# Kernel tuning notes

Measured on AMD Instinct MI355X. Metric: run time of the kernel, lower is better.

The kernel has to match this reference:

```python
import jax, jax.numpy as jnp
import numpy as np

N = 200000
E = 3200000
C = 64


def setup_inputs() -> dict:
    key = jax.random.key(0)
    ks = jax.random.split(key, 7)
    x = jax.random.normal(ks[0], (N, C), dtype=jnp.float32)
    sources = jax.random.randint(ks[1], (E,), 0, N, dtype=jnp.int32)
    targets = jax.random.randint(ks[2], (E,), 0, N, dtype=jnp.int32)
    norm = jax.random.uniform(ks[3], (N, 1), dtype=jnp.float32)
    norm_t = jax.random.uniform(ks[4], (N, 1), dtype=jnp.float32)
    # xavier_normal for [64,64] Linear: std = sqrt(2/(fan_in+fan_out))
    std = np.sqrt(2.0 / (C + C)).astype(np.float32)
    W_out = jax.random.normal(ks[5], (C, C), dtype=jnp.float32) * std
    W_back = jax.random.normal(ks[6], (C, C), dtype=jnp.float32) * std
    return {"x": x, "sources": sources, "targets": targets,
            "norm": norm, "norm_t": norm_t, "W_out": W_out, "W_back": W_back}


def _conv(x, src, dst, norm, W):
    # torch index_add: agg = x + scatter_add(x[src] -> dst)
    agg = x.at[dst].add(x[src])          # [N, C]
    y = norm * agg                       # [N, C] (norm broadcast [N,1])
    return jax.nn.relu(y @ W.T)          # Linear(bias=False): y @ W^T


def reference(x, sources, targets, norm, norm_t, W_out, W_back):
    out = _conv(x, sources, targets, norm, W_out)
    back = _conv(x, targets, sources, norm_t, W_back)
    return out + back
```

## Files before the change

kernel.cpp:

```cpp
#include <hip/hip_runtime.h>

#define NN 200000
#define CC 64
#define EE 3200000

#define SCAN_BLK 256
#define SCAN_ITEMS 4
#define SCAN_CHUNK (SCAN_BLK * SCAN_ITEMS)
#define NB ((NN + SCAN_CHUNK - 1) / SCAN_CHUNK)
static_assert(NB <= SCAN_BLK, "partials must fit one block");

__global__ void __launch_bounds__(256) count_kernel(
    const int* __restrict__ src, const int* __restrict__ dst,
    int* __restrict__ deg1, int* __restrict__ deg2)
{
    int e = blockIdx.x * blockDim.x + threadIdx.x;
    if (e >= EE) return;
    atomicAdd(&deg1[dst[e]], 1);
    atomicAdd(&deg2[src[e]], 1);
}

__global__ void __launch_bounds__(SCAN_BLK) reduce_kernel(
    const int* __restrict__ deg1, const int* __restrict__ deg2,
    int* __restrict__ p1, int* __restrict__ p2)
{
    __shared__ int s1[SCAN_BLK], s2[SCAN_BLK];
    int t = threadIdx.x, b = blockIdx.x;
    int base = b * SCAN_CHUNK + t * SCAN_ITEMS;
    int a = 0, c = 0;
    #pragma unroll
    for (int k = 0; k < SCAN_ITEMS; ++k) {
        int i = base + k;
        if (i < NN) { a += deg1[i]; c += deg2[i]; }
    }
    s1[t] = a; s2[t] = c; __syncthreads();
    for (int ofs = SCAN_BLK / 2; ofs > 0; ofs >>= 1) {
        if (t < ofs) { s1[t] += s1[t + ofs]; s2[t] += s2[t + ofs]; }
        __syncthreads();
    }
    if (t == 0) { p1[b] = s1[0]; p2[b] = s2[0]; }
}

__global__ void __launch_bounds__(SCAN_BLK) scanp_kernel(
    int* __restrict__ p1, int* __restrict__ p2)
{
    __shared__ int s[SCAN_BLK];
    int t = threadIdx.x;

    int v = (t < NB) ? p1[t] : 0;
    s[t] = v; __syncthreads();
    for (int ofs = 1; ofs < SCAN_BLK; ofs <<= 1) {
        int nv = (t >= ofs) ? s[t - ofs] : 0; __syncthreads();
        s[t] += nv; __syncthreads();
    }
    if (t < NB) p1[t] = s[t] - v;
    __syncthreads();

    v = (t < NB) ? p2[t] : 0;
    s[t] = v; __syncthreads();
    for (int ofs = 1; ofs < SCAN_BLK; ofs <<= 1) {
        int nv = (t >= ofs) ? s[t - ofs] : 0; __syncthreads();
        s[t] += nv; __syncthreads();
    }
    if (t < NB) p2[t] = s[t] - v;
}

__global__ void __launch_bounds__(SCAN_BLK) offsets_kernel(
    const int* __restrict__ deg1, const int* __restrict__ deg2,
    const int* __restrict__ p1, const int* __restrict__ p2,
    int* __restrict__ off1, int* __restrict__ off2,
    int* __restrict__ cur1, int* __restrict__ cur2)
{
    __shared__ int s[SCAN_BLK];
    int t = threadIdx.x, b = blockIdx.x;
    int base = b * SCAN_CHUNK + t * SCAN_ITEMS;

    {
        int d[SCAN_ITEMS]; int sum = 0;
        #pragma unroll
        for (int k = 0; k < SCAN_ITEMS; ++k) {
            int i = base + k;
            d[k] = (i < NN) ? deg1[i] : 0;
            sum += d[k];
        }
        s[t] = sum; __syncthreads();
        for (int ofs = 1; ofs < SCAN_BLK; ofs <<= 1) {
            int nv = (t >= ofs) ? s[t - ofs] : 0; __syncthreads();
            s[t] += nv; __syncthreads();
        }
        int run = s[t] - sum + p1[b];
        #pragma unroll
        for (int k = 0; k < SCAN_ITEMS; ++k) {
            int i = base + k;
            if (i < NN) { off1[i] = run; cur1[i] = run; }
            run += d[k];
        }
    }
    __syncthreads();
    {
        int d[SCAN_ITEMS]; int sum = 0;
        #pragma unroll
        for (int k = 0; k < SCAN_ITEMS; ++k) {
            int i = base + k;
            d[k] = (i < NN) ? deg2[i] : 0;
            sum += d[k];
        }
        s[t] = sum; __syncthreads();
        for (int ofs = 1; ofs < SCAN_BLK; ofs <<= 1) {
            int nv = (t >= ofs) ? s[t - ofs] : 0; __syncthreads();
            s[t] += nv; __syncthreads();
        }
        int run = s[t] - sum + p2[b];
        #pragma unroll
        for (int k = 0; k < SCAN_ITEMS; ++k) {
            int i = base + k;
            if (i < NN) { off2[i] = run; cur2[i] = run; }
            run += d[k];
        }
    }
}

__global__ void __launch_bounds__(256) fill_kernel(
    const int* __restrict__ src, const int* __restrict__ dst,
    int* __restrict__ cur1, int* __restrict__ cur2,
    int* __restrict__ adj1, int* __restrict__ adj2)
{
    int e = blockIdx.x * blockDim.x + threadIdx.x;
    if (e >= EE) return;
    int s = src[e], t = dst[e];
    int p = atomicAdd(&cur1[t], 1); adj1[p] = s;
    int q = atomicAdd(&cur2[s], 1); adj2[q] = t;
}

__global__ void __launch_bounds__(256) gather_gemm_kernel(
    const float* __restrict__ x,
    const int* __restrict__ off1, const int* __restrict__ deg1, const int* __restrict__ adj1,
    const int* __restrict__ off2, const int* __restrict__ deg2, const int* __restrict__ adj2,
    const float* __restrict__ norm, const float* __restrict__ norm_t,
    const float* __restrict__ Wo, const float* __restrict__ Wb,
    float* __restrict__ out)
{
    __shared__ float WoT[CC * CC];
    __shared__ float WbT[CC * CC];
    for (int idx = threadIdx.x; idx < CC * CC; idx += blockDim.x) {
        int j = idx >> 6, c = idx & 63;
        WoT[c * CC + j] = Wo[idx];
        WbT[c * CC + j] = Wb[idx];
    }
    __syncthreads();

    const int wave       = threadIdx.x >> 6;
    const int lane       = threadIdx.x & 63;
    const int wavesTotal = (gridDim.x * blockDim.x) >> 6;

    for (int i = blockIdx.x * (blockDim.x >> 6) + wave; i < NN; i += wavesTotal) {
        size_t base = (size_t)i * CC + lane;
        float xv = x[base];
        float a1 = xv, a2 = xv;

        {
            int st = off1[i], d = deg1[i];
            for (int b0 = 0; b0 < d; b0 += 64) {
                int cnt  = min(64, d - b0);
                int midx = (lane < cnt) ? adj1[st + b0 + lane] : 0;
                int k = 0;
                for (; k + 3 < cnt; k += 4) {
                    int n0 = __shfl(midx, k, 64),     n1 = __shfl(midx, k + 1, 64);
                    int n2 = __shfl(midx, k + 2, 64), n3 = __shfl(midx, k + 3, 64);
                    float v0 = x[(size_t)n0 * CC + lane];
                    float v1 = x[(size_t)n1 * CC + lane];
                    float v2 = x[(size_t)n2 * CC + lane];
                    float v3 = x[(size_t)n3 * CC + lane];
                    a1 += (v0 + v1) + (v2 + v3);
                }
                for (; k < cnt; ++k) {
                    int nb = __shfl(midx, k, 64);
                    a1 += x[(size_t)nb * CC + lane];
                }
            }
        }
        {
            int st = off2[i], d = deg2[i];
            for (int b0 = 0; b0 < d; b0 += 64) {
                int cnt  = min(64, d - b0);
                int midx = (lane < cnt) ? adj2[st + b0 + lane] : 0;
                int k = 0;
                for (; k + 3 < cnt; k += 4) {
                    int n0 = __shfl(midx, k, 64),     n1 = __shfl(midx, k + 1, 64);
                    int n2 = __shfl(midx, k + 2, 64), n3 = __shfl(midx, k + 3, 64);
                    float v0 = x[(size_t)n0 * CC + lane];
                    float v1 = x[(size_t)n1 * CC + lane];
                    float v2 = x[(size_t)n2 * CC + lane];
                    float v3 = x[(size_t)n3 * CC + lane];
                    a2 += (v0 + v1) + (v2 + v3);
                }
                for (; k < cnt; ++k) {
                    int nb = __shfl(midx, k, 64);
                    a2 += x[(size_t)nb * CC + lane];
                }
            }
        }

        float y1 = norm[i]   * a1;
        float y2 = norm_t[i] * a2;
        float acc1 = 0.f, acc2 = 0.f;
        #pragma unroll
        for (int c = 0; c < CC; ++c) {
            acc1 = fmaf(__shfl(y1, c, 64), WoT[c * CC + lane], acc1);
            acc2 = fmaf(__shfl(y2, c, 64), WbT[c * CC + lane], acc2);
        }
        out[base] = fmaxf(acc1, 0.f) + fmaxf(acc2, 0.f);
    }
}

__global__ void __launch_bounds__(256) scatter2_kernel(
    const float* __restrict__ x, const int* __restrict__ src, const int* __restrict__ dst,
    float* __restrict__ agg1, float* __restrict__ agg2)
{
    int tid = blockIdx.x * blockDim.x + threadIdx.x;
    int e = tid >> 6, lane = tid & 63;
    if (e >= EE) return;
    int s = src[e], t = dst[e];
    atomicAdd(&agg1[(size_t)t * CC + lane], x[(size_t)s * CC + lane]);
    atomicAdd(&agg2[(size_t)s * CC + lane], x[(size_t)t * CC + lane]);
}

__global__ void __launch_bounds__(256) gemm2_kernel(
    const float* __restrict__ x, const float* __restrict__ agg1, const float* __restrict__ agg2,
    const float* __restrict__ norm, const float* __restrict__ norm_t,
    const float* __restrict__ Wo, const float* __restrict__ Wb, float* __restrict__ out)
{
    __shared__ float WoT[CC * CC];
    __shared__ float WbT[CC * CC];
    for (int idx = threadIdx.x; idx < CC * CC; idx += blockDim.x) {
        int j = idx >> 6, c = idx & 63;
        WoT[c * CC + j] = Wo[idx];
        WbT[c * CC + j] = Wb[idx];
    }
    __syncthreads();
    const int wave = threadIdx.x >> 6, lane = threadIdx.x & 63;
    const int wavesTotal = (gridDim.x * blockDim.x) >> 6;
    for (int i = blockIdx.x * (blockDim.x >> 6) + wave; i < NN; i += wavesTotal) {
        size_t base = (size_t)i * CC + lane;
        float y1 = norm[i]   * (x[base] + agg1[base]);
        float y2 = norm_t[i] * (x[base] + agg2[base]);
        float acc1 = 0.f, acc2 = 0.f;
        #pragma unroll
        for (int c = 0; c < CC; ++c) {
            acc1 = fmaf(__shfl(y1, c, 64), WoT[c * CC + lane], acc1);
            acc2 = fmaf(__shfl(y2, c, 64), WbT[c * CC + lane], acc2);
        }
        out[base] = fmaxf(acc1, 0.f) + fmaxf(acc2, 0.f);
    }
}

extern "C" void kernel_launch(void* const* d_in, const int* in_sizes, int n_in,
                              void* d_out, int out_size, void* d_ws, size_t ws_size,
                              hipStream_t stream) {
    const float* x      = (const float*)d_in[0];
    const int*   src    = (const int*)  d_in[1];
    const int*   dst    = (const int*)  d_in[2];
    const float* norm   = (const float*)d_in[3];
    const float* norm_t = (const float*)d_in[4];
    const float* W_out  = (const float*)d_in[5];
    const float* W_back = (const float*)d_in[6];
    float*       out    = (float*)d_out;

    const size_t csrInts = (size_t)6 * NN + 512 + (size_t)2 * EE;
    if (ws_size >= csrInts * sizeof(int)) {
        int* deg1 = (int*)d_ws;
        int* deg2 = deg1 + NN;
        int* off1 = deg2 + NN;
        int* off2 = off1 + NN;
        int* cur1 = off2 + NN;
        int* cur2 = cur1 + NN;
        int* p1   = cur2 + NN;
        int* p2   = p1 + 256;
        int* adj1 = p2 + 256;
        int* adj2 = adj1 + EE;

        hipMemsetAsync(deg1, 0, 2 * NN * sizeof(int), stream);
        count_kernel<<<(EE + 255) / 256, 256, 0, stream>>>(src, dst, deg1, deg2);
        reduce_kernel<<<NB, SCAN_BLK, 0, stream>>>(deg1, deg2, p1, p2);
        scanp_kernel<<<1, SCAN_BLK, 0, stream>>>(p1, p2);
        offsets_kernel<<<NB, SCAN_BLK, 0, stream>>>(deg1, deg2, p1, p2,
                                                    off1, off2, cur1, cur2);
        fill_kernel<<<(EE + 255) / 256, 256, 0, stream>>>(src, dst, cur1, cur2, adj1, adj2);
        gather_gemm_kernel<<<2048, 256, 0, stream>>>(x, off1, deg1, adj1,
                                                     off2, deg2, adj2,
                                                     norm, norm_t, W_out, W_back, out);
    } else {
        const size_t aggElems = (size_t)NN * CC;
        float* agg1 = (float*)d_ws;
        float* agg2 = agg1 + aggElems;
        hipMemsetAsync(d_ws, 0, 2 * aggElems * sizeof(float), stream);
        scatter2_kernel<<<(EE * 64) / 256, 256, 0, stream>>>(x, src, dst, agg1, agg2);
        gemm2_kernel<<<4096, 256, 0, stream>>>(x, agg1, agg2, norm, norm_t,
                                               W_out, W_back, out);
    }
}
```

Baseline: 1.698 ms.

## Gather neighbor features from a bf16 copy of x with 16-byte loads

Adds a kernel that converts x to bf16 once per call, then a new gather+GEMM kernel. In it, 8 lanes each load 16 bytes of a neighbor row, so one wave gathers 8 neighbors at a time, and both edge directions are processed in one interleaved loop. The aim is to halve gather bandwidth and issue fewer, wider memory requests. The cost is bf16 rounding of neighbor features (the self term stays fp32), an extra conversion pass, and cross-lane reductions.

```diff
diff --git a/kernel.cpp b/kernel.cpp
--- a/kernel.cpp
+++ b/kernel.cpp
@@ -9,6 +9,26 @@
 #define SCAN_CHUNK (SCAN_BLK * SCAN_ITEMS)
 #define NB ((NN + SCAN_CHUNK - 1) / SCAN_CHUNK)
 static_assert(NB <= SCAN_BLK, "partials must fit one block");
+
+__device__ __forceinline__ unsigned int bf16rne(float f) {
+    unsigned int u = __float_as_uint(f);
+    return (u + 0x7fffu + ((u >> 16) & 1u)) >> 16;
+}
+
+__global__ void __launch_bounds__(256) tobf16_kernel(
+    const float* __restrict__ x, unsigned short* __restrict__ xh)
+{
+    int t = blockIdx.x * blockDim.x + threadIdx.x;
+    if (t >= NN * CC / 8) return;
+    const float4* x4 = (const float4*)x;
+    float4 f0 = x4[2 * t], f1 = x4[2 * t + 1];
+    int4 o;
+    o.x = (int)(bf16rne(f0.x) | (bf16rne(f0.y) << 16));
+    o.y = (int)(bf16rne(f0.z) | (bf16rne(f0.w) << 16));
+    o.z = (int)(bf16rne(f1.x) | (bf16rne(f1.y) << 16));
+    o.w = (int)(bf16rne(f1.z) | (bf16rne(f1.w) << 16));
+    ((int4*)xh)[t] = o;
+}
 
 __global__ void __launch_bounds__(256) count_kernel(
     const int* __restrict__ src, const int* __restrict__ dst,
@@ -132,6 +152,99 @@
     int q = atomicAdd(&cur2[s], 1); adj2[q] = t;
 }
 
+__device__ __forceinline__ void acc_bf8(const int4 u, float a[8]) {
+    unsigned int w;
+    w = (unsigned int)u.x; a[0] += __uint_as_float(w << 16); a[1] += __uint_as_float(w & 0xffff0000u);
+    w = (unsigned int)u.y; a[2] += __uint_as_float(w << 16); a[3] += __uint_as_float(w & 0xffff0000u);
+    w = (unsigned int)u.z; a[4] += __uint_as_float(w << 16); a[5] += __uint_as_float(w & 0xffff0000u);
+    w = (unsigned int)u.w; a[6] += __uint_as_float(w << 16); a[7] += __uint_as_float(w & 0xffff0000u);
+}
+
+__global__ void __launch_bounds__(256) gather_gemm_bf16_kernel(
+    const float* __restrict__ x,
+    const unsigned short* __restrict__ xh,
+    const int* __restrict__ off1, const int* __restrict__ deg1, const int* __restrict__ adj1,
+    const int* __restrict__ off2, const int* __restrict__ deg2, const int* __restrict__ adj2,
+    const float* __restrict__ norm, const float* __restrict__ norm_t,
+    const float* __restrict__ Wo, const float* __restrict__ Wb,
+    float* __restrict__ out)
+{
+    __shared__ float WoT[CC * CC];
+    __shared__ float WbT[CC * CC];
+    for (int idx = threadIdx.x; idx < CC * CC; idx += blockDim.x) {
+        int j = idx >> 6, c = idx & 63;
+        WoT[c * CC + j] = Wo[idx];
+        WbT[c * CC + j] = Wb[idx];
+    }
+    __syncthreads();
+
+    const int wave       = threadIdx.x >> 6;
+    const int lane       = threadIdx.x & 63;
+    const int g          = lane >> 3;
+    const int l          = lane & 7;
+    const int wavesTotal = (gridDim.x * blockDim.x) >> 6;
+    const int4* xh4      = (const int4*)xh;
+
+    for (int i = blockIdx.x * (blockDim.x >> 6) + wave; i < NN; i += wavesTotal) {
+        float a1[8], a2[8];
+        #pragma unroll
+        for (int t = 0; t < 8; ++t) { a1[t] = 0.f; a2[t] = 0.f; }
+
+        int d1 = deg1[i], st1 = off1[i];
+        int d2 = deg2[i], st2 = off2[i];
+        int dmax = max(d1, d2);
+
+        for (int b0 = 0; b0 < dmax; b0 += 64) {
+            int c1 = min(d1 - b0, 64);
+            int c2 = min(d2 - b0, 64);
+            int i1 = (lane < c1) ? adj1[st1 + b0 + lane] : 0;
+            int i2 = (lane < c2) ? adj2[st2 + b0 + lane] : 0;
+            int kmax = max(c1, c2);
+            #pragma unroll 2
+            for (int k = 0; k < kmax; k += 8) {
+                int j  = k + g;
+                int n1 = __shfl(i1, j, 64);
+                int n2 = __shfl(i2, j, 64);
+                if (j < c1) { int4 u = xh4[(size_t)n1 * 8 + l]; acc_bf8(u, a1); }
+                if (j < c2) { int4 u = xh4[(size_t)n2 * 8 + l]; acc_bf8(u, a2); }
+            }
+        }
+
+        #pragma unroll
+        for (int t = 0; t < 8; ++t) {
+            a1[t] += __shfl_xor(a1[t], 8, 64);
+            a1[t] += __shfl_xor(a1[t], 16, 64);
+            a1[t] += __shfl_xor(a1[t], 32, 64);
+            a2[t] += __shfl_xor(a2[t], 8, 64);
+            a2[t] += __shfl_xor(a2[t], 16, 64);
+            a2[t] += __shfl_xor(a2[t], 32, 64);
+        }
+
+        {
+            const float4* x4 = (const float4*)x;
+            float4 s0 = x4[(size_t)i * 16 + 2 * l];
+            float4 s1 = x4[(size_t)i * 16 + 2 * l + 1];
+            a1[0] += s0.x; a1[1] += s0.y; a1[2] += s0.z; a1[3] += s0.w;
+            a1[4] += s1.x; a1[5] += s1.y; a1[6] += s1.z; a1[7] += s1.w;
+            a2[0] += s0.x; a2[1] += s0.y; a2[2] += s0.z; a2[3] += s0.w;
+            a2[4] += s1.x; a2[5] += s1.y; a2[6] += s1.z; a2[7] += s1.w;
+        }
+
+        float nrm  = norm[i];
+        float nrmt = norm_t[i];
+        #pragma unroll
+        for (int t = 0; t < 8; ++t) { a1[t] *= nrm; a2[t] *= nrmt; }
+
+        float acc1 = 0.f, acc2 = 0.f;
+        #pragma unroll
+        for (int c = 0; c < CC; ++c) {
+            acc1 = fmaf(__shfl(a1[c & 7], c >> 3, 64), WoT[c * CC + lane], acc1);
+            acc2 = fmaf(__shfl(a2[c & 7], c >> 3, 64), WbT[c * CC + lane], acc2);
+        }
+        out[(size_t)i * CC + lane] = fmaxf(acc1, 0.f) + fmaxf(acc2, 0.f);
+    }
+}
+
 __global__ void __launch_bounds__(256) gather_gemm_kernel(
     const float* __restrict__ x,
     const int* __restrict__ off1, const int* __restrict__ deg1, const int* __restrict__ adj1,
@@ -148,61 +261,31 @@
         WbT[c * CC + j] = Wb[idx];
     }
     __syncthreads();
-
-    const int wave       = threadIdx.x >> 6;
-    const int lane       = threadIdx.x & 63;
+    const int wave = threadIdx.x >> 6, lane = threadIdx.x & 63;
     const int wavesTotal = (gridDim.x * blockDim.x) >> 6;
-
     for (int i = blockIdx.x * (blockDim.x >> 6) + wave; i < NN; i += wavesTotal) {
         size_t base = (size_t)i * CC + lane;
         float xv = x[base];
         float a1 = xv, a2 = xv;
-
         {
             int st = off1[i], d = deg1[i];
             for (int b0 = 0; b0 < d; b0 += 64) {
-                int cnt  = min(64, d - b0);
+                int cnt = min(64, d - b0);
                 int midx = (lane < cnt) ? adj1[st + b0 + lane] : 0;
-                int k = 0;
-                for (; k + 3 < cnt; k += 4) {
-                    int n0 = __shfl(midx, k, 64),     n1 = __shfl(midx, k + 1, 64);
-                    int n2 = __shfl(midx, k + 2, 64), n3 = __shfl(midx, k + 3, 64);
-                    float v0 = x[(size_t)n0 * CC + lane];
-                    float v1 = x[(size_t)n1 * CC + lane];
-                    float v2 = x[(size_t)n2 * CC + lane];
-                    float v3 = x[(size_t)n3 * CC + lane];
-                    a1 += (v0 + v1) + (v2 + v3);
-                }
-                for (; k < cnt; ++k) {
-                    int nb = __shfl(midx, k, 64);
-                    a1 += x[(size_t)nb * CC + lane];
-                }
+                for (int k = 0; k < cnt; ++k)
+                    a1 += x[(size_t)__shfl(midx, k, 64) * CC + lane];
             }
         }
         {
             int st = off2[i], d = deg2[i];
             for (int b0 = 0; b0 < d; b0 += 64) {
-                int cnt  = min(64, d - b0);
+                int cnt = min(64, d - b0);
                 int midx = (lane < cnt) ? adj2[st + b0 + lane] : 0;
-                int k = 0;
-                for (; k + 3 < cnt; k += 4) {
-                    int n0 = __shfl(midx, k, 64),     n1 = __shfl(midx, k + 1, 64);
-                    int n2 = __shfl(midx, k + 2, 64), n3 = __shfl(midx, k + 3, 64);
-                    float v0 = x[(size_t)n0 * CC + lane];
-                    float v1 = x[(size_t)n1 * CC + lane];
-                    float v2 = x[(size_t)n2 * CC + lane];
-                    float v3 = x[(size_t)n3 * CC + lane];
-                    a2 += (v0 + v1) + (v2 + v3);
-                }
-                for (; k < cnt; ++k) {
-                    int nb = __shfl(midx, k, 64);
-                    a2 += x[(size_t)nb * CC + lane];
-                }
+                for (int k = 0; k < cnt; ++k)
+                    a2 += x[(size_t)__shfl(midx, k, 64) * CC + lane];
             }
         }
-
-        float y1 = norm[i]   * a1;
-        float y2 = norm_t[i] * a2;
+        float y1 = norm[i] * a1, y2 = norm_t[i] * a2;
         float acc1 = 0.f, acc2 = 0.f;
         #pragma unroll
         for (int c = 0; c < CC; ++c) {
@@ -266,8 +349,36 @@
     const float* W_back = (const float*)d_in[6];
     float*       out    = (float*)d_out;
 
-    const size_t csrInts = (size_t)6 * NN + 512 + (size_t)2 * EE;
-    if (ws_size >= csrInts * sizeof(int)) {
+    const size_t xhBytes  = (size_t)NN * CC * 2;
+    const size_t csrInts  = (size_t)6 * NN + 512 + (size_t)2 * EE;
+    const size_t fullNeed = xhBytes + csrInts * sizeof(int);
+
+    if (ws_size >= fullNeed) {
+        unsigned short* xh = (unsigned short*)d_ws;
+        int* deg1 = (int*)((char*)d_ws + xhBytes);
+        int* deg2 = deg1 + NN;
+        int* off1 = deg2 + NN;
+        int* off2 = off1 + NN;
+        int* cur1 = off2 + NN;
+        int* cur2 = cur1 + NN;
+        int* p1   = cur2 + NN;
+        int* p2   = p1 + 256;
+        int* adj1 = p2 + 256;
+        int* adj2 = adj1 + EE;
+
+        hipMemsetAsync(deg1, 0, 2 * NN * sizeof(int), stream);
+        tobf16_kernel<<<(NN * CC / 8 + 255) / 256, 256, 0, stream>>>(x, xh);
+        count_kernel<<<(EE + 255) / 256, 256, 0, stream>>>(src, dst, deg1, deg2);
+        reduce_kernel<<<NB, SCAN_BLK, 0, stream>>>(deg1, deg2, p1, p2);
+        scanp_kernel<<<1, SCAN_BLK, 0, stream>>>(p1, p2);
+        offsets_kernel<<<NB, SCAN_BLK, 0, stream>>>(deg1, deg2, p1, p2,
+                                                    off1, off2, cur1, cur2);
+        fill_kernel<<<(EE + 255) / 256, 256, 0, stream>>>(src, dst, cur1, cur2, adj1, adj2);
+        gather_gemm_bf16_kernel<<<3072, 256, 0, stream>>>(x, xh,
+                                                          off1, deg1, adj1,
+                                                          off2, deg2, adj2,
+                                                          norm, norm_t, W_out, W_back, out);
+    } else if (ws_size >= csrInts * sizeof(int)) {
         int* deg1 = (int*)d_ws;
         int* deg2 = deg1 + NN;
         int* off1 = deg2 + NN;
```

After: 1.523 ms. 10.3% less time.
